# Optimization experiments

Hardware: AMD Instinct MI355X
Metric: run time of the kernel (lower is better)

The kernel has to match this reference:

```python
import jax, jax.numpy as jnp
import numpy as np

L, H = 6, 8          # n_layer, n_head
LN_EPS = 1e-5


def _ln(x, g, b):
    mu = jnp.mean(x, axis=-1, keepdims=True)
    var = jnp.mean((x - mu) ** 2, axis=-1, keepdims=True)
    return (x - mu) * jax.lax.rsqrt(var + LN_EPS) * g + b


def setup_inputs() -> dict:
    key = jax.random.key(0)
    B, T, V, D = 2, 2048, 32000, 512
    F = 4 * D
    std = 0.02
    ks = jax.random.split(key, 8)
    idx = jax.random.randint(ks[0], (B, T), 0, V)
    wte = jax.random.normal(ks[1], (V, D), dtype=jnp.float32) * std
    wpe = jax.random.normal(ks[2], (T, D), dtype=jnp.float32) * std
    qkv_w = jax.random.normal(ks[3], (L, D, 3 * D), dtype=jnp.float32) * std
    proj_w = jax.random.normal(ks[4], (L, D, D), dtype=jnp.float32) * std
    fc1_w = jax.random.normal(ks[5], (L, D, F), dtype=jnp.float32) * std
    fc2_w = jax.random.normal(ks[6], (L, F, D), dtype=jnp.float32) * std
    return dict(
        idx=idx, wte=wte, wpe=wpe,
        ln1_g=jnp.ones((L, D), jnp.float32), ln1_b=jnp.zeros((L, D), jnp.float32),
        qkv_w=qkv_w, qkv_b=jnp.zeros((L, 3 * D), jnp.float32),
        proj_w=proj_w, proj_b=jnp.zeros((L, D), jnp.float32),
        ln2_g=jnp.ones((L, D), jnp.float32), ln2_b=jnp.zeros((L, D), jnp.float32),
        fc1_w=fc1_w, fc1_b=jnp.zeros((L, F), jnp.float32),
        fc2_w=fc2_w, fc2_b=jnp.zeros((L, D), jnp.float32),
        lnf_g=jnp.ones((D,), jnp.float32), lnf_b=jnp.zeros((D,), jnp.float32),
    )


def reference(idx, wte, wpe, ln1_g, ln1_b, qkv_w, qkv_b, proj_w, proj_b,
              ln2_g, ln2_b, fc1_w, fc1_b, fc2_w, fc2_b, lnf_g, lnf_b):
    B, T = idx.shape
    D = wte.shape[1]
    hd = D // H
    scale = 1.0 / jnp.sqrt(jnp.asarray(hd, wte.dtype))
    x = wte[idx] + wpe[:T]                      # [B,T,D]
    mask = jnp.tril(jnp.ones((T, T), dtype=bool))

    def block(x, p):
        g1, b1, Wqkv, bqkv, Wp, bp, g2, b2, W1, bf1, W2, bf2 = p
        h = _ln(x, g1, b1)
        qkv = h @ Wqkv + bqkv                   # [B,T,3D]
        q, k, v = jnp.split(qkv, 3, axis=-1)
        q = q.reshape(B, T, H, hd)
        k = k.reshape(B, T, H, hd)
        v = v.reshape(B, T, H, hd)
        att = jnp.einsum('bqhd,bkhd->bhqk', q, k) * scale
        att = jnp.where(mask, att, -jnp.inf)
        att = jax.nn.softmax(att, axis=-1)
        y = jnp.einsum('bhqk,bkhd->bqhd', att, v).reshape(B, T, D)
        x = x + y @ Wp + bp
        h = _ln(x, g2, b2)
        x = x + jax.nn.gelu(h @ W1 + bf1, approximate=False) @ W2 + bf2
        return x, None

    x, _ = jax.lax.scan(block, x, (ln1_g, ln1_b, qkv_w, qkv_b, proj_w, proj_b,
                                   ln2_g, ln2_b, fc1_w, fc1_b, fc2_w, fc2_b))
    x = _ln(x, lnf_g, lnf_b)
    logits = x @ wte.T                          # tied head, [B,T,V]
    return logits
```

## Files before the change

kernel.cpp:

```cpp
#include <hip/hip_runtime.h>
#include <hip/hip_bf16.h>
#include <math.h>

#define BB 2
#define TT 2048
#define DD 512
#define HH 8
#define HD 64
#define FF 2048
#define VV 32000
#define LL 6
#define MM (BB * TT)

typedef unsigned int   u32;
typedef unsigned short u16;
typedef __attribute__((ext_vector_type(8))) short short8;
typedef __attribute__((ext_vector_type(4))) float f32x4;

__device__ __forceinline__ u16 f2bf_bits(float f)
{
    __hip_bfloat16 h = __float2bfloat16(f);
    u16 u;
    __builtin_memcpy(&u, &h, 2);
    return u;
}

__device__ __forceinline__ void gll16(const u16* g, u16* l)
{
    __builtin_amdgcn_global_load_lds(
        (const __attribute__((address_space(1))) u32*)g,
        (__attribute__((address_space(3))) u32*)l,
        16, 0, 0);
}

__device__ __forceinline__ float gelu_exact(float v)
{
    return 0.5f * v * (1.0f + erff(v * 0.70710678118654752440f));
}

__device__ __forceinline__ u16* swp(u16* base, int row, int col)
{
    int off = (row * 128 + col * 2) ^ ((row & 7) << 4);
    return (u16*)((char*)base + off);
}
__device__ __forceinline__ const u16* swpc(const u16* base, int row, int col)
{
    int off = (row * 128 + col * 2) ^ ((row & 7) << 4);
    return (const u16*)((const char*)base + off);
}

__global__ __launch_bounds__(128)
void embed_kernel(const int* __restrict__ idx, const float* __restrict__ wte,
                  const float* __restrict__ wpe, float* __restrict__ x)
{
    int row = blockIdx.x;
    int t = row & (TT - 1);
    int tok = idx[row];
    const float4* wt = (const float4*)(wte + (size_t)tok * DD);
    const float4* wp = (const float4*)(wpe + (size_t)t * DD);
    float4 a = wt[threadIdx.x];
    float4 p = wp[threadIdx.x];
    float4 r;
    r.x = a.x + p.x; r.y = a.y + p.y; r.z = a.z + p.z; r.w = a.w + p.w;
    ((float4*)(x + (size_t)row * DD))[threadIdx.x] = r;
}

__global__ __launch_bounds__(256)
void ln_kernel(const float* __restrict__ x, const float* __restrict__ g,
               const float* __restrict__ b, u16* __restrict__ out)
{
    int row = blockIdx.x;
    const float* xr = x + (size_t)row * DD;
    int tid = threadIdx.x;
    float v1 = xr[tid], v2 = xr[tid + 256];
    float s = v1 + v2;
    float ss = v1 * v1 + v2 * v2;
    #pragma unroll
    for (int o = 32; o; o >>= 1) {
        s  += __shfl_xor(s, o);
        ss += __shfl_xor(ss, o);
    }
    __shared__ float sred[4], ssred[4];
    int wid = tid >> 6, lane = tid & 63;
    if (lane == 0) { sred[wid] = s; ssred[wid] = ss; }
    __syncthreads();
    s  = sred[0] + sred[1] + sred[2] + sred[3];
    ss = ssred[0] + ssred[1] + ssred[2] + ssred[3];
    float mu  = s * (1.0f / DD);
    float var = ss * (1.0f / DD) - mu * mu;
    float rs  = rsqrtf(var + 1e-5f);
    u16* orow = out + (size_t)row * DD;
    orow[tid]       = f2bf_bits((v1 - mu) * rs * g[tid]       + b[tid]);
    orow[tid + 256] = f2bf_bits((v2 - mu) * rs * g[tid + 256] + b[tid + 256]);
}

__global__ __launch_bounds__(256)
void weight_prep_kernel(const float* __restrict__ qkv_w, const float* __restrict__ proj_w,
                        const float* __restrict__ fc1_w, const float* __restrict__ fc2_w,
                        u16* __restrict__ wqa, u16* __restrict__ wpa,
                        u16* __restrict__ w1a, u16* __restrict__ w2a)
{
    int id = blockIdx.x;
    int l = id / 3072, r = id % 3072;
    const float* in; u16* out; int K, N, tt;
    if (r < 768)       { in = qkv_w + (size_t)l * DD * 3 * DD; out = wqa + (size_t)l * 3 * DD * DD; K = DD; N = 3 * DD; tt = r; }
    else if (r < 1024) { in = proj_w + (size_t)l * DD * DD;    out = wpa + (size_t)l * DD * DD;    K = DD; N = DD;     tt = r - 768; }
    else if (r < 2048) { in = fc1_w + (size_t)l * DD * FF;     out = w1a + (size_t)l * DD * FF;    K = DD; N = FF;     tt = r - 1024; }
    else               { in = fc2_w + (size_t)l * FF * DD;     out = w2a + (size_t)l * FF * DD;    K = FF; N = DD;     tt = r - 2048; }
    int ntx = N >> 5;
    int n0 = (tt % ntx) << 5, k0 = (tt / ntx) << 5;
    __shared__ float tile[32][33];
    int tx = threadIdx.x & 31, ty = threadIdx.x >> 5;
    #pragma unroll
    for (int i = 0; i < 4; ++i)
        tile[ty + i * 8][tx] = in[(size_t)(k0 + ty + i * 8) * N + n0 + tx];
    __syncthreads();
    #pragma unroll
    for (int i = 0; i < 4; ++i)
        out[(size_t)(n0 + ty + i * 8) * K + k0 + tx] = f2bf_bits(tile[tx][ty + i * 8]);
}

__global__ __launch_bounds__(256)
void cvt_kernel(const float* __restrict__ in, u16* __restrict__ out, int n4)
{
    int i = blockIdx.x * 256 + threadIdx.x;
    if (i >= n4) return;
    float4 v = ((const float4*)in)[i];
    ushort4 o;
    o.x = f2bf_bits(v.x); o.y = f2bf_bits(v.y);
    o.z = f2bf_bits(v.z); o.w = f2bf_bits(v.w);
    ((ushort4*)out)[i] = o;
}

template<int BN, bool GELU_ACT, bool RESID, bool OUTBF16, bool QKV_SPLIT>
__global__ __launch_bounds__(256)
void mfma_gemm(const u16* __restrict__ A, const u16* __restrict__ Bt,
               const float* __restrict__ bias, const float* __restrict__ resid,
               void* __restrict__ Cout, u16* __restrict__ Vout,
               int M, int N, int K)
{
    constexpr int NJ = BN / 32;
    __shared__ u16 As[128 * 64];
    __shared__ u16 Bs[BN * 64];

    const int tid  = threadIdx.x;
    const int lane = tid & 63;
    const int w    = tid >> 6;
    const int wr   = w >> 1, wc = w & 1;

    const int nbx = gridDim.x;
    const int nwg = nbx * gridDim.y;
    int bid = blockIdx.y * nbx + blockIdx.x;
    int swz = (bid & 7) * (nwg >> 3) + (bid >> 3);
    const int m0 = (swz / nbx) * 128;
    const int n0 = (swz % nbx) * BN;

    const int trow = tid >> 3;
    const int tcol = (tid & 7) * 8;
    const u16* ga = A  + (size_t)(m0 + trow) * K + tcol;
    const u16* gb = Bt + (size_t)(n0 + trow) * K + tcol;
    u16* la = As + tid * 8;
    u16* lb = Bs + tid * 8;

    f32x4 acc[4][NJ] = {};

    const int fr = lane & 15;
    const int fk = (lane >> 4) * 8;

    for (int k0 = 0; k0 < K; k0 += 64) {
        #pragma unroll
        for (int p = 0; p < 4; ++p)
            gll16(ga + k0 + (size_t)p * 32 * K, la + p * 2048);
        #pragma unroll
        for (int p = 0; p < NJ; ++p)
            gll16(gb + k0 + (size_t)p * 32 * K, lb + p * 2048);
        asm volatile("s_waitcnt vmcnt(0)" ::: "memory");
        __syncthreads();

        #pragma unroll
        for (int ks = 0; ks < 2; ++ks) {
            short8 af[4], bfr[NJ];
            #pragma unroll
            for (int f = 0; f < 4; ++f)
                af[f]  = *(const short8*)&As[(wr * 64 + f * 16 + fr) * 64 + ks * 32 + fk];
            #pragma unroll
            for (int f = 0; f < NJ; ++f)
                bfr[f] = *(const short8*)&Bs[(wc * (BN / 2) + f * 16 + fr) * 64 + ks * 32 + fk];
            #pragma unroll
            for (int i = 0; i < 4; ++i)
                #pragma unroll
                for (int j = 0; j < NJ; ++j)
                    acc[i][j] = __builtin_amdgcn_mfma_f32_16x16x32_bf16(
                        af[i], bfr[j], acc[i][j], 0, 0, 0);
        }
        __syncthreads();
    }

    const int c0 = n0 + wc * (BN / 2) + fr;
    const int r0 = m0 + wr * 64 + ((lane >> 4) << 2);
    #pragma unroll
    for (int j = 0; j < NJ; ++j) {
        const int c = c0 + j * 16;
        const float bv = bias ? bias[c] : 0.0f;
        #pragma unroll
        for (int i = 0; i < 4; ++i) {
            #pragma unroll
            for (int r = 0; r < 4; ++r) {
                const int row = r0 + i * 16 + r;
                float v = acc[i][j][r] + bv;
                if constexpr (GELU_ACT) v = gelu_exact(v);
                if constexpr (RESID) v += resid[(size_t)row * N + c];
                if constexpr (QKV_SPLIT) {
                    if (c < 1024) {
                        ((u16*)Cout)[(size_t)row * 1024 + c] = f2bf_bits(v);
                    } else {
                        const int t = row & (TT - 1);
                        Vout[(((size_t)(row >> 11) * 512 + (c - 1024)) << 11) + t] = f2bf_bits(v);
                    }
                } else if constexpr (OUTBF16) {
                    ((u16*)Cout)[(size_t)row * N + c] = f2bf_bits(v);
                } else {
                    ((float*)Cout)[(size_t)row * N + c] = v;
                }
            }
        }
    }
}

__global__ __launch_bounds__(256)
void attn_kernel(const u16* __restrict__ qkb, const u16* __restrict__ vtb,
                 u16* __restrict__ y)
{
    const int l = blockIdx.x;
    const int u = l & 255, v = l >> 8;
    const int bh = u & 15;
    const int half = u >> 4;
    const int qt = v ? (16 + half) : (15 - half);
    const int h = bh & (HH - 1);
    const int b = bh >> 3;

    __shared__ alignas(16) u16 Qs[4096];
    __shared__ alignas(16) u16 Ks[2][4096];
    __shared__ alignas(16) u16 Vt[2][4096];
    __shared__ alignas(16) u16 Ps[4096];

    const int tid = threadIdx.x;
    const int lane = tid & 63;
    const int w = tid >> 6;
    const int ln = lane & 15, hi = lane >> 4;
    const int q0 = qt * 64;

    const u16* base  = qkb + (size_t)b * TT * 1024 + h * HD;
    const u16* vbase = vtb + (size_t)(b * 512 + h * HD) * TT;

    const int sr = tid >> 2, sc = (tid & 3) * 16;

    {
        const u16* qrow = base + (size_t)(q0 + sr) * 1024;
        *(short8*)swp(Qs, sr, sc)     = *(const short8*)(qrow + sc);
        *(short8*)swp(Qs, sr, sc + 8) = *(const short8*)(qrow + sc + 8);
    }
    short8 rk0, rk1, rv0, rv1;
    {
        const u16* krow = base + (size_t)sr * 1024 + 512;
        rk0 = *(const short8*)(krow + sc);
        rk1 = *(const short8*)(krow + sc + 8);
        const u16* vrow = vbase + (size_t)sr * TT;
        rv0 = *(const short8*)(vrow + sc);
        rv1 = *(const short8*)(vrow + sc + 8);
    }

    float m[4], lsum[4];
    f32x4 oacc[4] = {};
    #pragma unroll
    for (int r = 0; r < 4; ++r) { m[r] = -INFINITY; lsum[r] = 0.0f; }

    for (int kt = 0; kt <= qt; ++kt) {
        u16* ks = Ks[kt & 1];
        u16* vt = Vt[kt & 1];

        *(short8*)swp(ks, sr, sc)     = rk0;
        *(short8*)swp(ks, sr, sc + 8) = rk1;
        *(short8*)swp(vt, sr, sc)     = rv0;
        *(short8*)swp(vt, sr, sc + 8) = rv1;
        __syncthreads();

        if (kt < qt) {
            const int k0n = (kt + 1) * 64;
            const u16* krow = base + (size_t)(k0n + sr) * 1024 + 512;
            rk0 = *(const short8*)(krow + sc);
            rk1 = *(const short8*)(krow + sc + 8);
            const u16* vrow = vbase + (size_t)sr * TT + k0n;
            rv0 = *(const short8*)(vrow + sc);
            rv1 = *(const short8*)(vrow + sc + 8);
        }

        short8 aq[2];
        #pragma unroll
        for (int s2 = 0; s2 < 2; ++s2)
            aq[s2] = *(const short8*)swpc(Qs, w * 16 + ln, s2 * 32 + hi * 8);

        f32x4 sacc[4] = {};
        __builtin_amdgcn_s_setprio(1);
        #pragma unroll
        for (int j = 0; j < 4; ++j)
            #pragma unroll
            for (int s2 = 0; s2 < 2; ++s2) {
                short8 bk = *(const short8*)swpc(ks, j * 16 + ln, s2 * 32 + hi * 8);
                sacc[j] = __builtin_amdgcn_mfma_f32_16x16x32_bf16(aq[s2], bk, sacc[j], 0, 0, 0);
            }
        __builtin_amdgcn_s_setprio(0);

        const bool diag = (kt == qt);
        #pragma unroll
        for (int r = 0; r < 4; ++r) {
            const int qrow = w * 16 + hi * 4 + r;
            float sv[4];
            #pragma unroll
            for (int j = 0; j < 4; ++j) {
                float s = sacc[j][r] * 0.125f;
                if (diag && (j * 16 + ln > qrow)) s = -INFINITY;
                sv[j] = s;
            }
            float rm = fmaxf(fmaxf(sv[0], sv[1]), fmaxf(sv[2], sv[3]));
            #pragma unroll
            for (int o = 1; o < 16; o <<= 1) rm = fmaxf(rm, __shfl_xor(rm, o));
            float mn = fmaxf(m[r], rm);
            float corr = __expf(m[r] - mn);
            m[r] = mn;
            float ps = 0.0f;
            #pragma unroll
            for (int j = 0; j < 4; ++j) {
                float p = __expf(sv[j] - mn);
                ps += p;
                *swp(Ps, qrow, j * 16 + ln) = f2bf_bits(p);
            }
            #pragma unroll
            for (int o = 1; o < 16; o <<= 1) ps += __shfl_xor(ps, o);
            lsum[r] = lsum[r] * corr + ps;
            #pragma unroll
            for (int db = 0; db < 4; ++db) oacc[db][r] *= corr;
        }

        short8 ap[2];
        #pragma unroll
        for (int s2 = 0; s2 < 2; ++s2)
            ap[s2] = *(const short8*)swpc(Ps, w * 16 + ln, s2 * 32 + hi * 8);
        __builtin_amdgcn_s_setprio(1);
        #pragma unroll
        for (int db = 0; db < 4; ++db)
            #pragma unroll
            for (int s2 = 0; s2 < 2; ++s2) {
                short8 bv = *(const short8*)swpc(vt, db * 16 + ln, s2 * 32 + hi * 8);
                oacc[db] = __builtin_amdgcn_mfma_f32_16x16x32_bf16(ap[s2], bv, oacc[db], 0, 0, 0);
            }
        __builtin_amdgcn_s_setprio(0);
    }

    #pragma unroll
    for (int r = 0; r < 4; ++r) {
        const int q = q0 + w * 16 + hi * 4 + r;
        const float inv = 1.0f / lsum[r];
        u16* yrow = y + (size_t)(b * TT + q) * DD + h * HD;
        #pragma unroll
        for (int db = 0; db < 4; ++db)
            yrow[db * 16 + ln] = f2bf_bits(oacc[db][r] * inv);
    }
}

extern "C" void kernel_launch(void* const* d_in, const int* in_sizes, int n_in,
                              void* d_out, int out_size, void* d_ws, size_t ws_size,
                              hipStream_t stream)
{
    const int*   idx    = (const int*)  d_in[0];
    const float* wte    = (const float*)d_in[1];
    const float* wpe    = (const float*)d_in[2];
    const float* ln1_g  = (const float*)d_in[3];
    const float* ln1_b  = (const float*)d_in[4];
    const float* qkv_w  = (const float*)d_in[5];
    const float* qkv_b  = (const float*)d_in[6];
    const float* proj_w = (const float*)d_in[7];
    const float* proj_b = (const float*)d_in[8];
    const float* ln2_g  = (const float*)d_in[9];
    const float* ln2_b  = (const float*)d_in[10];
    const float* fc1_w  = (const float*)d_in[11];
    const float* fc1_b  = (const float*)d_in[12];
    const float* fc2_w  = (const float*)d_in[13];
    const float* fc2_b  = (const float*)d_in[14];
    const float* lnf_g  = (const float*)d_in[15];
    const float* lnf_b  = (const float*)d_in[16];
    float* out = (float*)d_out;

    char* ws = (char*)d_ws;
    float* x    = (float*)(ws);
    u16*   h    = (u16*)(ws + ((size_t)8  << 20));
    u16*   y    = (u16*)(ws + ((size_t)12 << 20));
    u16*   qkb  = (u16*)(ws + ((size_t)16 << 20));
    u16*   vtb  = (u16*)(ws + ((size_t)24 << 20));
    u16*   wqa  = (u16*)(ws + ((size_t)28 << 20));
    u16*   wpa  = (u16*)(ws + ((size_t)38 << 20));
    u16*   w1a  = (u16*)(ws + ((size_t)42 << 20));
    u16*   w2a  = (u16*)(ws + ((size_t)55 << 20));
    u16*   ffb  = (u16*)(ws + ((size_t)68 << 20));
    u16*   wteb = (u16*)(ws + ((size_t)85 << 20));

    embed_kernel<<<MM, 128, 0, stream>>>(idx, wte, wpe, x);

    weight_prep_kernel<<<LL * 3072, 256, 0, stream>>>(
        qkv_w, proj_w, fc1_w, fc2_w, wqa, wpa, w1a, w2a);

    cvt_kernel<<<(VV * DD / 4 + 255) / 256, 256, 0, stream>>>(wte, wteb, VV * DD / 4);

    for (int l = 0; l < LL; ++l) {
        ln_kernel<<<MM, 256, 0, stream>>>(x, ln1_g + l * DD, ln1_b + l * DD, h);

        mfma_gemm<128, false, false, true, true><<<dim3(12, 32), 256, 0, stream>>>(
            h, wqa + (size_t)l * 3 * DD * DD, qkv_b + (size_t)l * 3 * DD,
            nullptr, qkb, vtb, MM, 3 * DD, DD);

        attn_kernel<<<512, 256, 0, stream>>>(qkb, vtb, y);

        mfma_gemm<64, false, true, false, false><<<dim3(8, 32), 256, 0, stream>>>(
            y, wpa + (size_t)l * DD * DD, proj_b + (size_t)l * DD,
            x, x, nullptr, MM, DD, DD);

        ln_kernel<<<MM, 256, 0, stream>>>(x, ln2_g + l * DD, ln2_b + l * DD, h);

        mfma_gemm<128, true, false, true, false><<<dim3(16, 32), 256, 0, stream>>>(
            h, w1a + (size_t)l * DD * FF, fc1_b + (size_t)l * FF,
            nullptr, ffb, nullptr, MM, FF, DD);

        mfma_gemm<64, false, true, false, false><<<dim3(8, 32), 256, 0, stream>>>(
            ffb, w2a + (size_t)l * FF * DD, fc2_b + (size_t)l * DD,
            x, x, nullptr, MM, DD, FF);
    }

    ln_kernel<<<MM, 256, 0, stream>>>(x, lnf_g, lnf_b, h);

    mfma_gemm<128, false, false, false, false><<<dim3(250, 32), 256, 0, stream>>>(
        h, wteb, nullptr, nullptr, out, nullptr, MM, VV, DD);
}
```

Baseline: 1.195 ms.

## Double-buffer GEMM LDS tiles, vectorize V stores, streamline attention softmax

The GEMM now double-buffers its A/B shared-memory tiles so the next K-tile's global-to-LDS loads overlap the current tile's MFMA work, and it drops one barrier per iteration. The QKV-split epilogue writes transposed V as 4-wide vector stores. In attention, Q fragments are hoisted out of the key loop, exp is replaced by exp2 with log2e folded into the scale, and the per-row sum reduction across lanes is deferred to the end. The GEMM doubles its LDS footprint, which may lower occupancy, and correctness relies on the one remaining barrier ordering the buffer reuse.

New measurement: 1.159 ms (median of 2 runs). -3.0%, faster.

```diff
diff --git a/kernel.cpp b/kernel.cpp
--- a/kernel.cpp
+++ b/kernel.cpp
@@ -140,8 +140,8 @@
                int M, int N, int K)
 {
     constexpr int NJ = BN / 32;
-    __shared__ u16 As[128 * 64];
-    __shared__ u16 Bs[BN * 64];
+    __shared__ u16 As[2][128 * 64];
+    __shared__ u16 Bs[2][BN * 64];
 
     const int tid  = threadIdx.x;
     const int lane = tid & 63;
@@ -159,33 +159,41 @@
     const int tcol = (tid & 7) * 8;
     const u16* ga = A  + (size_t)(m0 + trow) * K + tcol;
     const u16* gb = Bt + (size_t)(n0 + trow) * K + tcol;
-    u16* la = As + tid * 8;
-    u16* lb = Bs + tid * 8;
+
+    auto stage = [&](int buf, int k0) {
+        u16* la = As[buf] + tid * 8;
+        u16* lb = Bs[buf] + tid * 8;
+        #pragma unroll
+        for (int p = 0; p < 4; ++p)
+            gll16(ga + k0 + (size_t)p * 32 * K, la + p * 2048);
+        #pragma unroll
+        for (int p = 0; p < NJ; ++p)
+            gll16(gb + k0 + (size_t)p * 32 * K, lb + p * 2048);
+    };
 
     f32x4 acc[4][NJ] = {};
 
     const int fr = lane & 15;
     const int fk = (lane >> 4) * 8;
 
-    for (int k0 = 0; k0 < K; k0 += 64) {
-        #pragma unroll
-        for (int p = 0; p < 4; ++p)
-            gll16(ga + k0 + (size_t)p * 32 * K, la + p * 2048);
-        #pragma unroll
-        for (int p = 0; p < NJ; ++p)
-            gll16(gb + k0 + (size_t)p * 32 * K, lb + p * 2048);
+    const int nt = K >> 6;
+    stage(0, 0);
+    for (int t = 0; t < nt; ++t) {
         asm volatile("s_waitcnt vmcnt(0)" ::: "memory");
         __syncthreads();
-
+        if (t + 1 < nt) stage((t + 1) & 1, (t + 1) << 6);
+
+        const u16* as = As[t & 1];
+        const u16* bs = Bs[t & 1];
         #pragma unroll
         for (int ks = 0; ks < 2; ++ks) {
             short8 af[4], bfr[NJ];
             #pragma unroll
             for (int f = 0; f < 4; ++f)
-                af[f]  = *(const short8*)&As[(wr * 64 + f * 16 + fr) * 64 + ks * 32 + fk];
+                af[f]  = *(const short8*)&as[(wr * 64 + f * 16 + fr) * 64 + ks * 32 + fk];
             #pragma unroll
             for (int f = 0; f < NJ; ++f)
-                bfr[f] = *(const short8*)&Bs[(wc * (BN / 2) + f * 16 + fr) * 64 + ks * 32 + fk];
+                bfr[f] = *(const short8*)&bs[(wc * (BN / 2) + f * 16 + fr) * 64 + ks * 32 + fk];
             #pragma unroll
             for (int i = 0; i < 4; ++i)
                 #pragma unroll
@@ -193,7 +201,6 @@
                     acc[i][j] = __builtin_amdgcn_mfma_f32_16x16x32_bf16(
                         af[i], bfr[j], acc[i][j], 0, 0, 0);
         }
-        __syncthreads();
     }
 
     const int c0 = n0 + wc * (BN / 2) + fr;
@@ -204,23 +211,33 @@
         const float bv = bias ? bias[c] : 0.0f;
         #pragma unroll
         for (int i = 0; i < 4; ++i) {
-            #pragma unroll
-            for (int r = 0; r < 4; ++r) {
-                const int row = r0 + i * 16 + r;
-                float v = acc[i][j][r] + bv;
-                if constexpr (GELU_ACT) v = gelu_exact(v);
-                if constexpr (RESID) v += resid[(size_t)row * N + c];
-                if constexpr (QKV_SPLIT) {
-                    if (c < 1024) {
-                        ((u16*)Cout)[(size_t)row * 1024 + c] = f2bf_bits(v);
-                    } else {
-                        const int t = row & (TT - 1);
-                        Vout[(((size_t)(row >> 11) * 512 + (c - 1024)) << 11) + t] = f2bf_bits(v);
-                    }
-                } else if constexpr (OUTBF16) {
-                    ((u16*)Cout)[(size_t)row * N + c] = f2bf_bits(v);
+            const int row0 = r0 + i * 16;
+            if constexpr (QKV_SPLIT) {
+                if (c < 1024) {
+                    #pragma unroll
+                    for (int r = 0; r < 4; ++r)
+                        ((u16*)Cout)[(size_t)(row0 + r) * 1024 + c] =
+                            f2bf_bits(acc[i][j][r] + bv);
                 } else {
-                    ((float*)Cout)[(size_t)row * N + c] = v;
+                    ushort4 o;
+                    o.x = f2bf_bits(acc[i][j][0] + bv);
+                    o.y = f2bf_bits(acc[i][j][1] + bv);
+                    o.z = f2bf_bits(acc[i][j][2] + bv);
+                    o.w = f2bf_bits(acc[i][j][3] + bv);
+                    const int t0 = row0 & (TT - 1);
+                    *(ushort4*)&Vout[(((size_t)(row0 >> 11) * 512 + (c - 1024)) << 11) + t0] = o;
+                }
+            } else {
+                #pragma unroll
+                for (int r = 0; r < 4; ++r) {
+                    const int row = row0 + r;
+                    float v = acc[i][j][r] + bv;
+                    if constexpr (GELU_ACT) v = gelu_exact(v);
+                    if constexpr (RESID) v += resid[(size_t)row * N + c];
+                    if constexpr (OUTBF16)
+                        ((u16*)Cout)[(size_t)row * N + c] = f2bf_bits(v);
+                    else
+                        ((float*)Cout)[(size_t)row * N + c] = v;
                 }
             }
         }
@@ -269,6 +286,12 @@
         rv0 = *(const short8*)(vrow + sc);
         rv1 = *(const short8*)(vrow + sc + 8);
     }
+    __syncthreads();
+
+    short8 aq0 = *(const short8*)swpc(Qs, w * 16 + ln, hi * 8);
+    short8 aq1 = *(const short8*)swpc(Qs, w * 16 + ln, 32 + hi * 8);
+
+    const float SC = 0.18033688011112042f;
 
     float m[4], lsum[4];
     f32x4 oacc[4] = {};
@@ -295,20 +318,15 @@
             rv1 = *(const short8*)(vrow + sc + 8);
         }
 
-        short8 aq[2];
-        #pragma unroll
-        for (int s2 = 0; s2 < 2; ++s2)
-            aq[s2] = *(const short8*)swpc(Qs, w * 16 + ln, s2 * 32 + hi * 8);
-
         f32x4 sacc[4] = {};
         __builtin_amdgcn_s_setprio(1);
         #pragma unroll
-        for (int j = 0; j < 4; ++j)
-            #pragma unroll
-            for (int s2 = 0; s2 < 2; ++s2) {
-                short8 bk = *(const short8*)swpc(ks, j * 16 + ln, s2 * 32 + hi * 8);
-                sacc[j] = __builtin_amdgcn_mfma_f32_16x16x32_bf16(aq[s2], bk, sacc[j], 0, 0, 0);
-            }
+        for (int j = 0; j < 4; ++j) {
+            short8 bk0 = *(const short8*)swpc(ks, j * 16 + ln, hi * 8);
+            short8 bk1 = *(const short8*)swpc(ks, j * 16 + ln, 32 + hi * 8);
+            sacc[j] = __builtin_amdgcn_mfma_f32_16x16x32_bf16(aq0, bk0, sacc[j], 0, 0, 0);
+            sacc[j] = __builtin_amdgcn_mfma_f32_16x16x32_bf16(aq1, bk1, sacc[j], 0, 0, 0);
+        }
         __builtin_amdgcn_s_setprio(0);
 
         const bool diag = (kt == qt);
@@ -318,7 +336,7 @@
             float sv[4];
             #pragma unroll
             for (int j = 0; j < 4; ++j) {
-                float s = sacc[j][r] * 0.125f;
+                float s = sacc[j][r] * SC;
                 if (diag && (j * 16 + ln > qrow)) s = -INFINITY;
                 sv[j] = s;
             }
@@ -326,41 +344,41 @@
             #pragma unroll
             for (int o = 1; o < 16; o <<= 1) rm = fmaxf(rm, __shfl_xor(rm, o));
             float mn = fmaxf(m[r], rm);
-            float corr = __expf(m[r] - mn);
+            float corr = exp2f(m[r] - mn);
             m[r] = mn;
-            float ps = 0.0f;
-            #pragma unroll
-            for (int j = 0; j < 4; ++j) {
-                float p = __expf(sv[j] - mn);
-                ps += p;
-                *swp(Ps, qrow, j * 16 + ln) = f2bf_bits(p);
-            }
-            #pragma unroll
-            for (int o = 1; o < 16; o <<= 1) ps += __shfl_xor(ps, o);
-            lsum[r] = lsum[r] * corr + ps;
+            float p0 = exp2f(sv[0] - mn);
+            float p1 = exp2f(sv[1] - mn);
+            float p2 = exp2f(sv[2] - mn);
+            float p3 = exp2f(sv[3] - mn);
+            *swp(Ps, qrow, ln)      = f2bf_bits(p0);
+            *swp(Ps, qrow, 16 + ln) = f2bf_bits(p1);
+            *swp(Ps, qrow, 32 + ln) = f2bf_bits(p2);
+            *swp(Ps, qrow, 48 + ln) = f2bf_bits(p3);
+            lsum[r] = lsum[r] * corr + ((p0 + p1) + (p2 + p3));
             #pragma unroll
             for (int db = 0; db < 4; ++db) oacc[db][r] *= corr;
         }
 
-        short8 ap[2];
-        #pragma unroll
-        for (int s2 = 0; s2 < 2; ++s2)
-            ap[s2] = *(const short8*)swpc(Ps, w * 16 + ln, s2 * 32 + hi * 8);
+        short8 ap0 = *(const short8*)swpc(Ps, w * 16 + ln, hi * 8);
+        short8 ap1 = *(const short8*)swpc(Ps, w * 16 + ln, 32 + hi * 8);
         __builtin_amdgcn_s_setprio(1);
         #pragma unroll
-        for (int db = 0; db < 4; ++db)
-            #pragma unroll
-            for (int s2 = 0; s2 < 2; ++s2) {
-                short8 bv = *(const short8*)swpc(vt, db * 16 + ln, s2 * 32 + hi * 8);
-                oacc[db] = __builtin_amdgcn_mfma_f32_16x16x32_bf16(ap[s2], bv, oacc[db], 0, 0, 0);
-            }
+        for (int db = 0; db < 4; ++db) {
+            short8 bv0 = *(const short8*)swpc(vt, db * 16 + ln, hi * 8);
+            short8 bv1 = *(const short8*)swpc(vt, db * 16 + ln, 32 + hi * 8);
+            oacc[db] = __builtin_amdgcn_mfma_f32_16x16x32_bf16(ap0, bv0, oacc[db], 0, 0, 0);
+            oacc[db] = __builtin_amdgcn_mfma_f32_16x16x32_bf16(ap1, bv1, oacc[db], 0, 0, 0);
+        }
         __builtin_amdgcn_s_setprio(0);
     }
 
     #pragma unroll
     for (int r = 0; r < 4; ++r) {
+        float lt = lsum[r];
+        #pragma unroll
+        for (int o = 1; o < 16; o <<= 1) lt += __shfl_xor(lt, o);
         const int q = q0 + w * 16 + hi * 4 + r;
-        const float inv = 1.0f / lsum[r];
+        const float inv = 1.0f / lt;
         u16* yrow = y + (size_t)(b * TT + q) * DD + h * HD;
         #pragma unroll
         for (int db = 0; db < 4; ++db)
```
